# Performance work log

Hardware: AMD Instinct MI355X
Metric: run time of the kernel (lower is better)

Reference implementation:

```python
import jax, jax.numpy as jnp
import numpy as np

WS = (2, 7, 7)  # window size (T, H, W)
NUM_HEADS = 8


def _relative_position_index():
    t, h, w = WS
    coords = np.stack(np.meshgrid(np.arange(t), np.arange(h), np.arange(w), indexing='ij'))  # (3,t,h,w)
    flat = coords.reshape(3, -1)  # (3, N)
    rel = flat[:, :, None] - flat[:, None, :]  # (3, N, N)
    rel = rel.transpose(1, 2, 0).astype(np.int32)  # (N, N, 3)
    rel[..., 0] += t - 1
    rel[..., 1] += h - 1
    rel[..., 2] += w - 1
    rel[..., 0] *= (2 * h - 1) * (2 * w - 1)
    rel[..., 1] *= 2 * w - 1
    return rel.sum(-1)  # (N, N)


def setup_inputs() -> dict:
    key = jax.random.key(0)
    ks = jax.random.split(key, 7)
    B_, N, C = 2048, 98, 256
    nW = 512
    table_size = (2 * WS[0] - 1) * (2 * WS[1] - 1) * (2 * WS[2] - 1)  # 507
    return {
        'x': jax.random.normal(ks[0], (B_, N, C), jnp.float32),
        'mask': jax.random.normal(ks[1], (nW, N, N), jnp.float32),
        'qkv_w': jax.random.normal(ks[2], (3 * C, C), jnp.float32) * 0.02,
        'qkv_b': jax.random.normal(ks[3], (3 * C,), jnp.float32) * 0.02,
        'proj_w': jax.random.normal(ks[4], (C, C), jnp.float32) * 0.02,
        'proj_b': jax.random.normal(ks[5], (C,), jnp.float32) * 0.02,
        'bias_table': jax.random.normal(ks[6], (table_size, NUM_HEADS), jnp.float32) * 0.02,
        'rel_index': jnp.asarray(_relative_position_index()),
    }


def reference(x, mask, qkv_w, qkv_b, proj_w, proj_b, bias_table, rel_index):
    B_, N, C = x.shape
    H = NUM_HEADS
    hd = C // H
    scale = hd ** -0.5
    # QKV projection -> (3, B_, H, N, hd)
    qkv = (x @ qkv_w.T + qkv_b).reshape(B_, N, 3, H, hd).transpose(2, 0, 3, 1, 4)
    q, k, v = qkv[0], qkv[1], qkv[2]
    attn = jnp.einsum('bhnd,bhmd->bhnm', q * scale, k)  # (B_, H, N, N)
    # gathered relative-position bias -> (H, N, N)
    bias = bias_table[rel_index.reshape(-1)].reshape(N, N, H).transpose(2, 0, 1)
    attn = attn + bias[None]
    nW = mask.shape[0]
    attn = attn.reshape(B_ // nW, nW, H, N, N) + mask[None, :, None]
    attn = jax.nn.softmax(attn.reshape(B_, H, N, N), axis=-1)
    out = jnp.einsum('bhnm,bhmd->bhnd', attn, v)  # (B_, H, N, hd)
    out = out.transpose(0, 2, 1, 3).reshape(B_, N, C)
    return out @ proj_w.T + proj_b
```

## Files before the change

kernel.cpp:

```cpp
#include <hip/hip_runtime.h>
#include <hip/hip_bf16.h>

typedef __attribute__((ext_vector_type(8))) short short8;
typedef __attribute__((ext_vector_type(4))) float f32x4;

__device__ __forceinline__ unsigned short f2bf(float f) {
    __hip_bfloat16 h = __float2bfloat16(f);
    union { __hip_bfloat16 h; unsigned short u; } c; c.h = h; return c.u;
}

typedef __attribute__((address_space(1))) const unsigned int gas_u32;
typedef __attribute__((address_space(3))) unsigned int las_u32;

__device__ __forceinline__ void gload_lds16(const unsigned short* g, unsigned short* l) {
    __builtin_amdgcn_global_load_lds((gas_u32*)g, (las_u32*)l, 16, 0, 0);
}

__global__ void cvt_bf16_kernel(const float* __restrict__ src,
                                unsigned short* __restrict__ dst, long n8) {
    long stride = (long)gridDim.x * 256;
    for (long t = (long)blockIdx.x * 256 + threadIdx.x; t < n8; t += stride) {
        long i = t * 8;
        float4 f0 = *reinterpret_cast<const float4*>(src + i);
        float4 f1 = *reinterpret_cast<const float4*>(src + i + 4);
        uint4 u;
        u.x = ((unsigned)f2bf(f0.y) << 16) | f2bf(f0.x);
        u.y = ((unsigned)f2bf(f0.w) << 16) | f2bf(f0.z);
        u.z = ((unsigned)f2bf(f1.y) << 16) | f2bf(f1.x);
        u.w = ((unsigned)f2bf(f1.w) << 16) | f2bf(f1.z);
        *reinterpret_cast<uint4*>(dst + i) = u;
    }
}

__global__ void bias_expand_kernel(const float* __restrict__ bias_table,
                                   const int* __restrict__ rel_index,
                                   float* __restrict__ bias_full) {
    int idx = blockIdx.x * 256 + threadIdx.x;
    if (idx >= 8 * 9604) return;
    int h = idx / 9604;
    int r = idx - h * 9604;
    bias_full[idx] = bias_table[rel_index[r] * 8 + h];
}

__global__ void vt_zerofill_kernel(unsigned short* __restrict__ vtws) {
    int idx = blockIdx.x * 256 + threadIdx.x;
    if (idx >= 16384 * 32 * 7) return;
    int bhd = idx / 7, j = idx - bhd * 7;
    unsigned* p = reinterpret_cast<unsigned*>(vtws + (long)bhd * 112 + 98);
    p[j] = 0;
}

__global__ __launch_bounds__(256, 4)
void gemm_qkv_kernel(const unsigned short* __restrict__ Xb,
                     const unsigned short* __restrict__ Wb,
                     const float* __restrict__ bias,
                     unsigned short* __restrict__ qws,
                     unsigned short* __restrict__ kws,
                     unsigned short* __restrict__ vtws) {
    __shared__ unsigned short As[128 * 64];
    __shared__ unsigned short Bs[128 * 64];
    const int tid = threadIdx.x;
    const int wave = tid >> 6, lane = tid & 63;
    const int q4 = lane >> 4, l16 = lane & 15;
    const int wr = wave >> 1, wc = wave & 1;

    const int nwg = gridDim.x * gridDim.y;
    const int bid = blockIdx.y * gridDim.x + blockIdx.x;
    const int swz = (bid & 7) * (nwg >> 3) + (bid >> 3);
    const int bx = swz % gridDim.x;
    const int by = swz / gridDim.x;

    const long m0 = (long)by * 128;
    const int n0 = bx * 128;

    const int srow = lane >> 3;
    const int scol = (lane & 7) << 3;

    f32x4 acc[4][4];
#pragma unroll
    for (int i = 0; i < 4; ++i)
#pragma unroll
        for (int j = 0; j < 4; ++j) acc[i][j] = (f32x4){0.f, 0.f, 0.f, 0.f};

    for (int ks = 0; ks < 256; ks += 64) {
#pragma unroll
        for (int i = 0; i < 4; ++i) {
            int c = wave * 4 + i;
            gload_lds16(Xb + (m0 + c * 8 + srow) * 256 + ks + scol, &As[c * 512]);
            gload_lds16(Wb + (long)(n0 + c * 8 + srow) * 256 + ks + scol, &Bs[c * 512]);
        }
        __syncthreads();
#pragma unroll
        for (int s = 0; s < 2; ++s) {
            short8 a[4], b[4];
#pragma unroll
            for (int i = 0; i < 4; ++i)
                a[i] = *reinterpret_cast<const short8*>(&As[(wr * 64 + i * 16 + l16) * 64 + s * 32 + q4 * 8]);
#pragma unroll
            for (int j = 0; j < 4; ++j)
                b[j] = *reinterpret_cast<const short8*>(&Bs[(wc * 64 + j * 16 + l16) * 64 + s * 32 + q4 * 8]);
#pragma unroll
            for (int i = 0; i < 4; ++i)
#pragma unroll
                for (int j = 0; j < 4; ++j)
                    acc[i][j] = __builtin_amdgcn_mfma_f32_16x16x32_bf16(a[i], b[j], acc[i][j], 0, 0, 0);
        }
        __syncthreads();
    }
#pragma unroll
    for (int i = 0; i < 4; ++i) {
#pragma unroll
        for (int r = 0; r < 4; ++r) {
            long row = m0 + wr * 64 + i * 16 + q4 * 4 + r;
            int b_ = (int)(row / 98);
            int n_ = (int)(row - (long)b_ * 98);
#pragma unroll
            for (int j = 0; j < 4; ++j) {
                int col = n0 + wc * 64 + j * 16 + l16;
                float vv = acc[i][j][r] + bias[col];
                int which = col >> 8;
                int h = (col >> 5) & 7;
                int d = col & 31;
                if (which == 2) {
                    vtws[((long)(b_ * 8 + h) * 32 + d) * 112 + n_] = f2bf(vv);
                } else {
                    unsigned short* dst = which ? kws : qws;
                    dst[((long)(b_ * 8 + h) * 98 + n_) * 32 + d] = f2bf(vv);
                }
            }
        }
    }
}

__global__ __launch_bounds__(256, 4)
void attn_kernel(const unsigned short* __restrict__ q,
                 const unsigned short* __restrict__ k,
                 const unsigned short* __restrict__ vt,
                 const float* __restrict__ mask,
                 const float* __restrict__ bias_full,
                 unsigned short* __restrict__ attn_out) {
    __shared__ unsigned short Qs[112 * 40];
    __shared__ unsigned short Ks[112 * 40];
    __shared__ unsigned short Vt[32 * 136];

    const int tid = threadIdx.x;
    const int wave = tid >> 6, lane = tid & 63;
    const int q4 = lane >> 4, l16 = lane & 15;
    const int bh = blockIdx.x;
    const int b = bh >> 3, h = bh & 7;
    const int w = b & 511;
    const long base = (long)bh * 98 * 32;

    for (int idx = tid; idx < 448; idx += 256) {
        int n = idx >> 2, dg = (idx & 3) * 8;
        uint4 val = make_uint4(0, 0, 0, 0);
        if (n < 98) val = *reinterpret_cast<const uint4*>(q + base + n * 32 + dg);
        *reinterpret_cast<uint4*>(&Qs[n * 40 + dg]) = val;
    }
    for (int idx = tid; idx < 448; idx += 256) {
        int n = idx >> 2, dg = (idx & 3) * 8;
        uint4 val = make_uint4(0, 0, 0, 0);
        if (n < 98) val = *reinterpret_cast<const uint4*>(k + base + n * 32 + dg);
        *reinterpret_cast<uint4*>(&Ks[n * 40 + dg]) = val;
    }
    const unsigned short* vtp = vt + (long)bh * 3584;
    for (int idx = tid; idx < 448; idx += 256) {
        int d = idx / 14, ch = idx - d * 14;
        *reinterpret_cast<uint4*>(&Vt[d * 136 + ch * 8]) =
            *reinterpret_cast<const uint4*>(vtp + d * 112 + ch * 8);
    }
    if (tid < 64) {
        int d = tid >> 1, c = tid & 1;
        *reinterpret_cast<uint4*>(&Vt[d * 136 + 112 + c * 8]) = make_uint4(0, 0, 0, 0);
    }
    __syncthreads();

    const float scale = 0.17677669529663687f;
    const float* maskp = mask + (long)w * 9604;
    const float* biasp = bias_full + (long)h * 9604;
    const long obase = (long)b * 98 * 256 + h * 32;

    for (int tr = wave; tr < 7; tr += 4) {
        const int n = tr * 16 + l16;
        short8 bq = *reinterpret_cast<const short8*>(&Qs[(tr * 16 + l16) * 40 + q4 * 8]);
        f32x4 pv[7];
#pragma unroll
        for (int i = 0; i < 7; ++i) {
            short8 ak = *reinterpret_cast<const short8*>(&Ks[(i * 16 + l16) * 40 + q4 * 8]);
            f32x4 d = (f32x4){0.f, 0.f, 0.f, 0.f};
            d = __builtin_amdgcn_mfma_f32_16x16x32_bf16(ak, bq, d, 0, 0, 0);
            int m0 = i * 16 + q4 * 4;
            f32x4 o;
            if (n < 98 && m0 + 3 < 98) {
                float2 mk0 = *reinterpret_cast<const float2*>(maskp + n * 98 + m0);
                float2 mk1 = *reinterpret_cast<const float2*>(maskp + n * 98 + m0 + 2);
                float2 bb0 = *reinterpret_cast<const float2*>(biasp + n * 98 + m0);
                float2 bb1 = *reinterpret_cast<const float2*>(biasp + n * 98 + m0 + 2);
                o[0] = d[0] * scale + mk0.x + bb0.x;
                o[1] = d[1] * scale + mk0.y + bb0.y;
                o[2] = d[2] * scale + mk1.x + bb1.x;
                o[3] = d[3] * scale + mk1.y + bb1.y;
            } else {
#pragma unroll
                for (int r = 0; r < 4; ++r) {
                    int m = m0 + r;
                    o[r] = (n < 98 && m < 98)
                         ? d[r] * scale + maskp[n * 98 + m] + biasp[n * 98 + m]
                         : -1e30f;
                }
            }
            pv[i] = o;
        }
        float mx = -1e30f;
#pragma unroll
        for (int i = 0; i < 7; ++i)
#pragma unroll
            for (int r = 0; r < 4; ++r) mx = fmaxf(mx, pv[i][r]);
        mx = fmaxf(mx, __shfl_xor(mx, 16));
        mx = fmaxf(mx, __shfl_xor(mx, 32));
        float sm = 0.f;
#pragma unroll
        for (int i = 0; i < 7; ++i)
#pragma unroll
            for (int r = 0; r < 4; ++r) {
                float e = __expf(pv[i][r] - mx);
                pv[i][r] = e;
                sm += e;
            }
        sm += __shfl_xor(sm, 16);
        sm += __shfl_xor(sm, 32);
        float rinv = 1.f / sm;
        unsigned up[8][2];
#pragma unroll
        for (int i = 0; i < 7; ++i) {
            up[i][0] = ((unsigned)f2bf(pv[i][1] * rinv) << 16) | f2bf(pv[i][0] * rinv);
            up[i][1] = ((unsigned)f2bf(pv[i][3] * rinv) << 16) | f2bf(pv[i][2] * rinv);
        }
        up[7][0] = 0; up[7][1] = 0;
        f32x4 o0 = (f32x4){0.f, 0.f, 0.f, 0.f};
        f32x4 o1 = (f32x4){0.f, 0.f, 0.f, 0.f};
        const int srcA = ((q4 & 1) * 2) * 16 + l16;
        const int srcB = srcA + 16;
        const bool hi = (q4 >= 2);
#pragma unroll
        for (int kc = 0; kc < 4; ++kc) {
            int ie = 2 * kc, io = 2 * kc + 1;
            unsigned a0e = __shfl(up[ie][0], srcA), a0o = __shfl(up[io][0], srcA);
            unsigned a1e = __shfl(up[ie][1], srcA), a1o = __shfl(up[io][1], srcA);
            unsigned b0e = __shfl(up[ie][0], srcB), b0o = __shfl(up[io][0], srcB);
            unsigned b1e = __shfl(up[ie][1], srcB), b1o = __shfl(up[io][1], srcB);
            union { uint4 u; short8 s; } cvt;
            cvt.u.x = hi ? a0o : a0e;
            cvt.u.y = hi ? a1o : a1e;
            cvt.u.z = hi ? b0o : b0e;
            cvt.u.w = hi ? b1o : b1e;
            short8 bv0 = *reinterpret_cast<const short8*>(&Vt[l16 * 136 + kc * 32 + q4 * 8]);
            short8 bv1 = *reinterpret_cast<const short8*>(&Vt[(16 + l16) * 136 + kc * 32 + q4 * 8]);
            o0 = __builtin_amdgcn_mfma_f32_16x16x32_bf16(cvt.s, bv0, o0, 0, 0, 0);
            o1 = __builtin_amdgcn_mfma_f32_16x16x32_bf16(cvt.s, bv1, o1, 0, 0, 0);
        }
#pragma unroll
        for (int r = 0; r < 4; ++r) {
            int nn = tr * 16 + q4 * 4 + r;
            if (nn < 98) {
                attn_out[obase + nn * 256 + l16] = f2bf(o0[r]);
                attn_out[obase + nn * 256 + 16 + l16] = f2bf(o1[r]);
            }
        }
    }
}

__global__ __launch_bounds__(256, 4)
void gemm_proj_kernel(const unsigned short* __restrict__ Abf,
                      const unsigned short* __restrict__ Wb,
                      const float* __restrict__ bias,
                      float* __restrict__ out) {
    __shared__ unsigned short As[128 * 64];
    __shared__ unsigned short Bs[128 * 64];
    const int tid = threadIdx.x;
    const int wave = tid >> 6, lane = tid & 63;
    const int q4 = lane >> 4, l16 = lane & 15;
    const int wr = wave >> 1, wc = wave & 1;

    const int nwg = gridDim.x * gridDim.y;
    const int bid = blockIdx.y * gridDim.x + blockIdx.x;
    const int swz = (bid & 7) * (nwg >> 3) + (bid >> 3);
    const int bx = swz % gridDim.x;
    const int by = swz / gridDim.x;

    const long m0 = (long)by * 128;
    const int n0 = bx * 128;

    const int srow = lane >> 3;
    const int scol = (lane & 7) << 3;

    f32x4 acc[4][4];
#pragma unroll
    for (int i = 0; i < 4; ++i)
#pragma unroll
        for (int j = 0; j < 4; ++j) acc[i][j] = (f32x4){0.f, 0.f, 0.f, 0.f};

    for (int ks = 0; ks < 256; ks += 64) {
#pragma unroll
        for (int i = 0; i < 4; ++i) {
            int c = wave * 4 + i;
            gload_lds16(Abf + (m0 + c * 8 + srow) * 256 + ks + scol, &As[c * 512]);
            gload_lds16(Wb + (long)(n0 + c * 8 + srow) * 256 + ks + scol, &Bs[c * 512]);
        }
        __syncthreads();
#pragma unroll
        for (int s = 0; s < 2; ++s) {
            short8 a[4], b[4];
#pragma unroll
            for (int i = 0; i < 4; ++i)
                a[i] = *reinterpret_cast<const short8*>(&As[(wr * 64 + i * 16 + l16) * 64 + s * 32 + q4 * 8]);
#pragma unroll
            for (int j = 0; j < 4; ++j)
                b[j] = *reinterpret_cast<const short8*>(&Bs[(wc * 64 + j * 16 + l16) * 64 + s * 32 + q4 * 8]);
#pragma unroll
            for (int i = 0; i < 4; ++i)
#pragma unroll
                for (int j = 0; j < 4; ++j)
                    acc[i][j] = __builtin_amdgcn_mfma_f32_16x16x32_bf16(a[i], b[j], acc[i][j], 0, 0, 0);
        }
        __syncthreads();
    }
#pragma unroll
    for (int i = 0; i < 4; ++i) {
#pragma unroll
        for (int r = 0; r < 4; ++r) {
            long row = m0 + wr * 64 + i * 16 + q4 * 4 + r;
#pragma unroll
            for (int j = 0; j < 4; ++j) {
                int col = n0 + wc * 64 + j * 16 + l16;
                out[row * 256 + col] = acc[i][j][r] + bias[col];
            }
        }
    }
}

extern "C" void kernel_launch(void* const* d_in, const int* in_sizes, int n_in,
                              void* d_out, int out_size, void* d_ws, size_t ws_size,
                              hipStream_t stream) {
    (void)in_sizes; (void)n_in; (void)out_size; (void)ws_size;
    const float* x          = (const float*)d_in[0];
    const float* mask       = (const float*)d_in[1];
    const float* qkv_w      = (const float*)d_in[2];
    const float* qkv_b      = (const float*)d_in[3];
    const float* proj_w     = (const float*)d_in[4];
    const float* proj_b     = (const float*)d_in[5];
    const float* bias_table = (const float*)d_in[6];
    const int*   rel_index  = (const int*)d_in[7];
    float* out = (float*)d_out;

    const long QN = 51380224;
    const long VT = 58720256;
    unsigned short* qws  = (unsigned short*)d_ws;
    unsigned short* kws  = qws + QN;
    unsigned short* vtws = kws + QN;
    unsigned short* aow  = vtws + VT;
    float* bias_full = (float*)(aow + QN);
    unsigned short* wqkvb  = (unsigned short*)(bias_full + 8 * 9604);
    unsigned short* wprojb = wqkvb + 768 * 256;
    unsigned short* xb = aow;

    vt_zerofill_kernel<<<dim3((16384 * 32 * 7 + 255) / 256), dim3(256), 0, stream>>>(vtws);
    bias_expand_kernel<<<dim3((8 * 9604 + 255) / 256), dim3(256), 0, stream>>>(
        bias_table, rel_index, bias_full);
    cvt_bf16_kernel<<<dim3(2048), dim3(256), 0, stream>>>(x, xb, 51380224L / 8);
    cvt_bf16_kernel<<<dim3(96), dim3(256), 0, stream>>>(qkv_w, wqkvb, 196608L / 8);
    cvt_bf16_kernel<<<dim3(32), dim3(256), 0, stream>>>(proj_w, wprojb, 65536L / 8);
    gemm_qkv_kernel<<<dim3(6, 1568), dim3(256), 0, stream>>>(
        xb, wqkvb, qkv_b, qws, kws, vtws);
    attn_kernel<<<dim3(16384), dim3(256), 0, stream>>>(
        qws, kws, vtws, mask, bias_full, aow);
    gemm_proj_kernel<<<dim3(2, 1568), dim3(256), 0, stream>>>(
        aow, wprojb, proj_b, out);
}
```

Measured before the change: 994.5 us.

## Pad mask/bias to 112, fold scale into Q, 7-wave attention blocks, XCD-aware ordering

Pre-pads the mask and relative-position bias to 112x112, with -1e30 in padded key columns, so the attention kernel can load them as aligned float4 without bounds checks. The softmax scale moves into the QKV GEMM epilogue. The attention block grows to 448 threads (7 waves, one 16-row tile each), which removes the strided tile loop and lets the staging loops run in a single pass. Block IDs are remapped so blocks that share a mask window land on the same XCD, improving L2 reuse of the mask. In exchange, an extra pre-pass writes a padded mask of about 25 MB each call.

```diff
diff --git a/kernel.cpp b/kernel.cpp
--- a/kernel.cpp
+++ b/kernel.cpp
@@ -32,14 +32,28 @@
     }
 }
 
-__global__ void bias_expand_kernel(const float* __restrict__ bias_table,
-                                   const int* __restrict__ rel_index,
-                                   float* __restrict__ bias_full) {
+__global__ void mask_pad_kernel(const float* __restrict__ mask,
+                                float* __restrict__ mask_pad) {
     int idx = blockIdx.x * 256 + threadIdx.x;
-    if (idx >= 8 * 9604) return;
-    int h = idx / 9604;
-    int r = idx - h * 9604;
-    bias_full[idx] = bias_table[rel_index[r] * 8 + h];
+    if (idx >= 512 * 12544) return;
+    int w = idx / 12544, rem = idx - w * 12544;
+    int n = rem / 112, m = rem - n * 112;
+    float v;
+    if (m >= 98) v = -1e30f;
+    else if (n >= 98) v = 0.f;
+    else v = mask[w * 9604 + n * 98 + m];
+    mask_pad[idx] = v;
+}
+
+__global__ void bias_pad_kernel(const float* __restrict__ bias_table,
+                                const int* __restrict__ rel_index,
+                                float* __restrict__ bias_pad) {
+    int idx = blockIdx.x * 256 + threadIdx.x;
+    if (idx >= 8 * 12544) return;
+    int h = idx / 12544, rem = idx - h * 12544;
+    int n = rem / 112, m = rem - n * 112;
+    float v = (n < 98 && m < 98) ? bias_table[rel_index[n * 98 + m] * 8 + h] : 0.f;
+    bias_pad[idx] = v;
 }
 
 __global__ void vt_zerofill_kernel(unsigned short* __restrict__ vtws) {
@@ -107,6 +121,7 @@
         }
         __syncthreads();
     }
+    const float scale = 0.17677669529663687f;
 #pragma unroll
     for (int i = 0; i < 4; ++i) {
 #pragma unroll
@@ -123,21 +138,22 @@
                 int d = col & 31;
                 if (which == 2) {
                     vtws[((long)(b_ * 8 + h) * 32 + d) * 112 + n_] = f2bf(vv);
+                } else if (which == 1) {
+                    kws[((long)(b_ * 8 + h) * 98 + n_) * 32 + d] = f2bf(vv);
                 } else {
-                    unsigned short* dst = which ? kws : qws;
-                    dst[((long)(b_ * 8 + h) * 98 + n_) * 32 + d] = f2bf(vv);
+                    qws[((long)(b_ * 8 + h) * 98 + n_) * 32 + d] = f2bf(vv * scale);
                 }
             }
         }
     }
 }
 
-__global__ __launch_bounds__(256, 4)
+__global__ __launch_bounds__(448, 7)
 void attn_kernel(const unsigned short* __restrict__ q,
                  const unsigned short* __restrict__ k,
                  const unsigned short* __restrict__ vt,
-                 const float* __restrict__ mask,
-                 const float* __restrict__ bias_full,
+                 const float* __restrict__ mask_pad,
+                 const float* __restrict__ bias_pad,
                  unsigned short* __restrict__ attn_out) {
     __shared__ unsigned short Qs[112 * 40];
     __shared__ unsigned short Ks[112 * 40];
@@ -146,26 +162,29 @@
     const int tid = threadIdx.x;
     const int wave = tid >> 6, lane = tid & 63;
     const int q4 = lane >> 4, l16 = lane & 15;
-    const int bh = blockIdx.x;
-    const int b = bh >> 3, h = bh & 7;
-    const int w = b & 511;
+
+    const int d0 = blockIdx.x;
+    const int xcd = d0 & 7, jj = d0 >> 3;
+    const int w = xcd * 64 + (jj >> 5);
+    const int sub = jj & 31;
+    const int b = (sub >> 3) * 512 + w;
+    const int h = sub & 7;
+    const int bh = b * 8 + h;
     const long base = (long)bh * 98 * 32;
 
-    for (int idx = tid; idx < 448; idx += 256) {
-        int n = idx >> 2, dg = (idx & 3) * 8;
-        uint4 val = make_uint4(0, 0, 0, 0);
-        if (n < 98) val = *reinterpret_cast<const uint4*>(q + base + n * 32 + dg);
-        *reinterpret_cast<uint4*>(&Qs[n * 40 + dg]) = val;
-    }
-    for (int idx = tid; idx < 448; idx += 256) {
-        int n = idx >> 2, dg = (idx & 3) * 8;
-        uint4 val = make_uint4(0, 0, 0, 0);
-        if (n < 98) val = *reinterpret_cast<const uint4*>(k + base + n * 32 + dg);
-        *reinterpret_cast<uint4*>(&Ks[n * 40 + dg]) = val;
-    }
-    const unsigned short* vtp = vt + (long)bh * 3584;
-    for (int idx = tid; idx < 448; idx += 256) {
-        int d = idx / 14, ch = idx - d * 14;
+    {
+        int n = tid >> 2, dg = (tid & 3) * 8;
+        uint4 vq = make_uint4(0, 0, 0, 0), vk = make_uint4(0, 0, 0, 0);
+        if (n < 98) {
+            vq = *reinterpret_cast<const uint4*>(q + base + n * 32 + dg);
+            vk = *reinterpret_cast<const uint4*>(k + base + n * 32 + dg);
+        }
+        *reinterpret_cast<uint4*>(&Qs[n * 40 + dg]) = vq;
+        *reinterpret_cast<uint4*>(&Ks[n * 40 + dg]) = vk;
+    }
+    {
+        const unsigned short* vtp = vt + (long)bh * 3584;
+        int d = tid / 14, ch = tid - d * 14;
         *reinterpret_cast<uint4*>(&Vt[d * 136 + ch * 8]) =
             *reinterpret_cast<const uint4*>(vtp + d * 112 + ch * 8);
     }
@@ -175,97 +194,83 @@
     }
     __syncthreads();
 
-    const float scale = 0.17677669529663687f;
-    const float* maskp = mask + (long)w * 9604;
-    const float* biasp = bias_full + (long)h * 9604;
+    const float* mp = mask_pad + (long)w * 12544;
+    const float* bp = bias_pad + (long)h * 12544;
     const long obase = (long)b * 98 * 256 + h * 32;
 
-    for (int tr = wave; tr < 7; tr += 4) {
-        const int n = tr * 16 + l16;
-        short8 bq = *reinterpret_cast<const short8*>(&Qs[(tr * 16 + l16) * 40 + q4 * 8]);
-        f32x4 pv[7];
-#pragma unroll
-        for (int i = 0; i < 7; ++i) {
-            short8 ak = *reinterpret_cast<const short8*>(&Ks[(i * 16 + l16) * 40 + q4 * 8]);
-            f32x4 d = (f32x4){0.f, 0.f, 0.f, 0.f};
-            d = __builtin_amdgcn_mfma_f32_16x16x32_bf16(ak, bq, d, 0, 0, 0);
-            int m0 = i * 16 + q4 * 4;
-            f32x4 o;
-            if (n < 98 && m0 + 3 < 98) {
-                float2 mk0 = *reinterpret_cast<const float2*>(maskp + n * 98 + m0);
-                float2 mk1 = *reinterpret_cast<const float2*>(maskp + n * 98 + m0 + 2);
-                float2 bb0 = *reinterpret_cast<const float2*>(biasp + n * 98 + m0);
-                float2 bb1 = *reinterpret_cast<const float2*>(biasp + n * 98 + m0 + 2);
-                o[0] = d[0] * scale + mk0.x + bb0.x;
-                o[1] = d[1] * scale + mk0.y + bb0.y;
-                o[2] = d[2] * scale + mk1.x + bb1.x;
-                o[3] = d[3] * scale + mk1.y + bb1.y;
-            } else {
-#pragma unroll
-                for (int r = 0; r < 4; ++r) {
-                    int m = m0 + r;
-                    o[r] = (n < 98 && m < 98)
-                         ? d[r] * scale + maskp[n * 98 + m] + biasp[n * 98 + m]
-                         : -1e30f;
-                }
-            }
-            pv[i] = o;
-        }
-        float mx = -1e30f;
-#pragma unroll
-        for (int i = 0; i < 7; ++i)
-#pragma unroll
-            for (int r = 0; r < 4; ++r) mx = fmaxf(mx, pv[i][r]);
-        mx = fmaxf(mx, __shfl_xor(mx, 16));
-        mx = fmaxf(mx, __shfl_xor(mx, 32));
-        float sm = 0.f;
-#pragma unroll
-        for (int i = 0; i < 7; ++i)
-#pragma unroll
-            for (int r = 0; r < 4; ++r) {
-                float e = __expf(pv[i][r] - mx);
-                pv[i][r] = e;
-                sm += e;
-            }
-        sm += __shfl_xor(sm, 16);
-        sm += __shfl_xor(sm, 32);
-        float rinv = 1.f / sm;
-        unsigned up[8][2];
-#pragma unroll
-        for (int i = 0; i < 7; ++i) {
-            up[i][0] = ((unsigned)f2bf(pv[i][1] * rinv) << 16) | f2bf(pv[i][0] * rinv);
-            up[i][1] = ((unsigned)f2bf(pv[i][3] * rinv) << 16) | f2bf(pv[i][2] * rinv);
-        }
-        up[7][0] = 0; up[7][1] = 0;
-        f32x4 o0 = (f32x4){0.f, 0.f, 0.f, 0.f};
-        f32x4 o1 = (f32x4){0.f, 0.f, 0.f, 0.f};
-        const int srcA = ((q4 & 1) * 2) * 16 + l16;
-        const int srcB = srcA + 16;
-        const bool hi = (q4 >= 2);
-#pragma unroll
-        for (int kc = 0; kc < 4; ++kc) {
-            int ie = 2 * kc, io = 2 * kc + 1;
-            unsigned a0e = __shfl(up[ie][0], srcA), a0o = __shfl(up[io][0], srcA);
-            unsigned a1e = __shfl(up[ie][1], srcA), a1o = __shfl(up[io][1], srcA);
-            unsigned b0e = __shfl(up[ie][0], srcB), b0o = __shfl(up[io][0], srcB);
-            unsigned b1e = __shfl(up[ie][1], srcB), b1o = __shfl(up[io][1], srcB);
-            union { uint4 u; short8 s; } cvt;
-            cvt.u.x = hi ? a0o : a0e;
-            cvt.u.y = hi ? a1o : a1e;
-            cvt.u.z = hi ? b0o : b0e;
-            cvt.u.w = hi ? b1o : b1e;
-            short8 bv0 = *reinterpret_cast<const short8*>(&Vt[l16 * 136 + kc * 32 + q4 * 8]);
-            short8 bv1 = *reinterpret_cast<const short8*>(&Vt[(16 + l16) * 136 + kc * 32 + q4 * 8]);
-            o0 = __builtin_amdgcn_mfma_f32_16x16x32_bf16(cvt.s, bv0, o0, 0, 0, 0);
-            o1 = __builtin_amdgcn_mfma_f32_16x16x32_bf16(cvt.s, bv1, o1, 0, 0, 0);
-        }
+    const int tr = wave;
+    const int n = tr * 16 + l16;
+    const float* mrow = mp + n * 112;
+    const float* brow = bp + n * 112;
+    short8 bq = *reinterpret_cast<const short8*>(&Qs[n * 40 + q4 * 8]);
+    f32x4 pv[7];
+#pragma unroll
+    for (int i = 0; i < 7; ++i) {
+        short8 ak = *reinterpret_cast<const short8*>(&Ks[(i * 16 + l16) * 40 + q4 * 8]);
+        f32x4 d = (f32x4){0.f, 0.f, 0.f, 0.f};
+        d = __builtin_amdgcn_mfma_f32_16x16x32_bf16(ak, bq, d, 0, 0, 0);
+        int m0 = i * 16 + q4 * 4;
+        float4 mk = *reinterpret_cast<const float4*>(mrow + m0);
+        float4 bb = *reinterpret_cast<const float4*>(brow + m0);
+        pv[i][0] = d[0] + mk.x + bb.x;
+        pv[i][1] = d[1] + mk.y + bb.y;
+        pv[i][2] = d[2] + mk.z + bb.z;
+        pv[i][3] = d[3] + mk.w + bb.w;
+    }
+    float mx = -1e30f;
+#pragma unroll
+    for (int i = 0; i < 7; ++i)
+#pragma unroll
+        for (int r = 0; r < 4; ++r) mx = fmaxf(mx, pv[i][r]);
+    mx = fmaxf(mx, __shfl_xor(mx, 16));
+    mx = fmaxf(mx, __shfl_xor(mx, 32));
+    float sm = 0.f;
+#pragma unroll
+    for (int i = 0; i < 7; ++i)
 #pragma unroll
         for (int r = 0; r < 4; ++r) {
-            int nn = tr * 16 + q4 * 4 + r;
-            if (nn < 98) {
-                attn_out[obase + nn * 256 + l16] = f2bf(o0[r]);
-                attn_out[obase + nn * 256 + 16 + l16] = f2bf(o1[r]);
-            }
+            float e = __expf(pv[i][r] - mx);
+            pv[i][r] = e;
+            sm += e;
+        }
+    sm += __shfl_xor(sm, 16);
+    sm += __shfl_xor(sm, 32);
+    float rinv = 1.f / sm;
+    unsigned up[8][2];
+#pragma unroll
+    for (int i = 0; i < 7; ++i) {
+        up[i][0] = ((unsigned)f2bf(pv[i][1] * rinv) << 16) | f2bf(pv[i][0] * rinv);
+        up[i][1] = ((unsigned)f2bf(pv[i][3] * rinv) << 16) | f2bf(pv[i][2] * rinv);
+    }
+    up[7][0] = 0; up[7][1] = 0;
+    f32x4 o0 = (f32x4){0.f, 0.f, 0.f, 0.f};
+    f32x4 o1 = (f32x4){0.f, 0.f, 0.f, 0.f};
+    const int srcA = ((q4 & 1) * 2) * 16 + l16;
+    const int srcB = srcA + 16;
+    const bool hi = (q4 >= 2);
+#pragma unroll
+    for (int kc = 0; kc < 4; ++kc) {
+        int ie = 2 * kc, io = 2 * kc + 1;
+        unsigned a0e = __shfl(up[ie][0], srcA), a0o = __shfl(up[io][0], srcA);
+        unsigned a1e = __shfl(up[ie][1], srcA), a1o = __shfl(up[io][1], srcA);
+        unsigned b0e = __shfl(up[ie][0], srcB), b0o = __shfl(up[io][0], srcB);
+        unsigned b1e = __shfl(up[ie][1], srcB), b1o = __shfl(up[io][1], srcB);
+        union { uint4 u; short8 s; } cvt;
+        cvt.u.x = hi ? a0o : a0e;
+        cvt.u.y = hi ? a1o : a1e;
+        cvt.u.z = hi ? b0o : b0e;
+        cvt.u.w = hi ? b1o : b1e;
+        short8 bv0 = *reinterpret_cast<const short8*>(&Vt[l16 * 136 + kc * 32 + q4 * 8]);
+        short8 bv1 = *reinterpret_cast<const short8*>(&Vt[(16 + l16) * 136 + kc * 32 + q4 * 8]);
+        o0 = __builtin_amdgcn_mfma_f32_16x16x32_bf16(cvt.s, bv0, o0, 0, 0, 0);
+        o1 = __builtin_amdgcn_mfma_f32_16x16x32_bf16(cvt.s, bv1, o1, 0, 0, 0);
+    }
+#pragma unroll
+    for (int r = 0; r < 4; ++r) {
+        int nn = tr * 16 + q4 * 4 + r;
+        if (nn < 98) {
+            attn_out[obase + nn * 256 + l16] = f2bf(o0[r]);
+            attn_out[obase + nn * 256 + 16 + l16] = f2bf(o1[r]);
         }
     }
 }
@@ -359,21 +364,24 @@
     unsigned short* kws  = qws + QN;
     unsigned short* vtws = kws + QN;
     unsigned short* aow  = vtws + VT;
-    float* bias_full = (float*)(aow + QN);
-    unsigned short* wqkvb  = (unsigned short*)(bias_full + 8 * 9604);
+    float* mask_padw = (float*)(aow + QN);
+    float* bias_padw = mask_padw + 512 * 12544;
+    unsigned short* wqkvb  = (unsigned short*)(bias_padw + 8 * 12544);
     unsigned short* wprojb = wqkvb + 768 * 256;
     unsigned short* xb = aow;
 
     vt_zerofill_kernel<<<dim3((16384 * 32 * 7 + 255) / 256), dim3(256), 0, stream>>>(vtws);
-    bias_expand_kernel<<<dim3((8 * 9604 + 255) / 256), dim3(256), 0, stream>>>(
-        bias_table, rel_index, bias_full);
+    mask_pad_kernel<<<dim3((512 * 12544 + 255) / 256), dim3(256), 0, stream>>>(
+        mask, mask_padw);
+    bias_pad_kernel<<<dim3((8 * 12544 + 255) / 256), dim3(256), 0, stream>>>(
+        bias_table, rel_index, bias_padw);
     cvt_bf16_kernel<<<dim3(2048), dim3(256), 0, stream>>>(x, xb, 51380224L / 8);
     cvt_bf16_kernel<<<dim3(96), dim3(256), 0, stream>>>(qkv_w, wqkvb, 196608L / 8);
     cvt_bf16_kernel<<<dim3(32), dim3(256), 0, stream>>>(proj_w, wprojb, 65536L / 8);
     gemm_qkv_kernel<<<dim3(6, 1568), dim3(256), 0, stream>>>(
         xb, wqkvb, qkv_b, qws, kws, vtws);
-    attn_kernel<<<dim3(16384), dim3(256), 0, stream>>>(
-        qws, kws, vtws, mask, bias_full, aow);
+    attn_kernel<<<dim3(16384), dim3(448), 0, stream>>>(
+        qws, kws, vtws, mask_padw, bias_padw, aow);
     gemm_proj_kernel<<<dim3(2, 1568), dim3(256), 0, stream>>>(
         aow, wprojb, proj_b, out);
 }
```

After: 922.1 us. 1.08x faster.
